# Optimization experiments

Measured on AMD Instinct MI355X. Metric: run time of the kernel, lower is better.

The kernel has to match this reference:

```python
import jax, jax.numpy as jnp
import numpy as np

B, IN_CH, OUT_CH = 4, 64, 128
N_HIGH, N_LOW = 163842, 40962
GROUPS, EPS, SLOPE = 4, 1e-5, 0.2


def setup_inputs() -> dict:
    key = jax.random.key(0)
    ks = jax.random.split(key, 6)
    x = jax.random.normal(ks[0], (B, IN_CH, N_HIGH), jnp.float32)
    pool_neigh = jax.random.randint(ks[1], (N_LOW * 7,), 0, N_HIGH, dtype=jnp.int32)
    conv_neigh = jax.random.randint(ks[2], (N_LOW * 7,), 0, N_LOW, dtype=jnp.int32)
    W1 = jax.random.normal(ks[3], (OUT_CH, 7 * IN_CH), jnp.float32) / np.float32(np.sqrt(7 * IN_CH))
    b1 = jnp.zeros((OUT_CH,), jnp.float32)
    W2 = jax.random.normal(ks[4], (OUT_CH, 7 * OUT_CH), jnp.float32) / np.float32(np.sqrt(7 * OUT_CH))
    b2 = jnp.zeros((OUT_CH,), jnp.float32)
    return dict(x=x, pool_neigh=pool_neigh, conv_neigh=conv_neigh,
                W1=W1, b1=b1, gn1_w=jnp.ones((OUT_CH,), jnp.float32), gn1_b=jnp.zeros((OUT_CH,), jnp.float32),
                W2=W2, b2=b2, gn2_w=jnp.ones((OUT_CH,), jnp.float32), gn2_b=jnp.zeros((OUT_CH,), jnp.float32))


def _mean_pool(x, pool_neigh):
    # x: (B, C, N_high); pool_neigh: (N_low*7,) -> (B, C, N_low)
    g = x[:, :, pool_neigh].reshape(x.shape[0], x.shape[1], -1, 7)
    return g.mean(axis=-1)


def _onering_conv(x, neigh, W, b):
    # x: (B, C, N); neigh: (N*7,); W: (O, 7*C). Torch Linear over gathered
    # (N*7, C).view(N, 7*C): neighbor-major, channel-minor concatenation.
    Bb, C, N = x.shape
    feat = x[:, :, neigh].reshape(Bb, C, N, 7)            # (B, C, N, 7)
    feat = jnp.transpose(feat, (0, 2, 3, 1)).reshape(Bb, N, 7 * C)  # (B, N, 7C)
    out = jnp.einsum('bnf,of->bno', feat, W) + b          # (B, N, O)
    return jnp.transpose(out, (0, 2, 1))                  # (B, O, N)


def _group_norm(x, w, b):
    # x: (B, C, N), normalize per (group, sample) over (C//G, N)
    Bb, C, N = x.shape
    xg = x.reshape(Bb, GROUPS, C // GROUPS, N)
    mu = xg.mean(axis=(2, 3), keepdims=True)
    var = ((xg - mu) ** 2).mean(axis=(2, 3), keepdims=True)
    xn = ((xg - mu) * jax.lax.rsqrt(var + EPS)).reshape(Bb, C, N)
    return xn * w[None, :, None] + b[None, :, None]


def _leaky_relu(x):
    return jnp.where(x >= 0, x, SLOPE * x)


def reference(x, pool_neigh, conv_neigh, W1, b1, gn1_w, gn1_b, W2, b2, gn2_w, gn2_b):
    h = _mean_pool(x, pool_neigh)
    h = _leaky_relu(_group_norm(_onering_conv(h, conv_neigh, W1, b1), gn1_w, gn1_b))
    h = _leaky_relu(_group_norm(_onering_conv(h, conv_neigh, W2, b2), gn2_w, gn2_b))
    return h
```

## Files before the change

### kernel.cpp

```cpp
#include <hip/hip_runtime.h>

#define B_SZ 4
#define IN_CH 64
#define OUT_CH 128
#define NHI 163842
#define NLO 40962
#define EPS_GN 1e-5f
#define SLOPE 0.2f

typedef __attribute__((ext_vector_type(8))) short short8;
typedef __attribute__((ext_vector_type(16))) float f32x16;

__device__ inline ushort f2bf(float f) {
    union { float f; unsigned u; } v; v.f = f;
    unsigned r = v.u + 0x7FFF + ((v.u >> 16) & 1);
    return (ushort)(r >> 16);
}
__device__ inline float bf2f(ushort h) {
    union { unsigned u; float f; } v; v.u = ((unsigned)h) << 16;
    return v.f;
}

__global__ void k_transpose_x(const float* __restrict__ x, ushort* __restrict__ xT) {
    __shared__ float t[64][65];
    const int b   = blockIdx.y;
    const int n0  = blockIdx.x * 64;
    const int tid = threadIdx.x;
    const int nq  = tid & 15;
    const int c0  = tid >> 4;
    const bool full = (n0 + 64) <= NHI;
    if (full) {
#pragma unroll
        for (int r = 0; r < 4; ++r) {
            int c = c0 + r * 16;
            float4 v = *(const float4*)&x[((long)b * IN_CH + c) * NHI + n0 + nq * 4];
            t[c][nq * 4 + 0] = v.x; t[c][nq * 4 + 1] = v.y;
            t[c][nq * 4 + 2] = v.z; t[c][nq * 4 + 3] = v.w;
        }
    } else {
        for (int r = 0; r < 4; ++r) {
            int c = c0 + r * 16;
            for (int e = 0; e < 4; ++e) {
                int n = n0 + nq * 4 + e;
                t[c][nq * 4 + e] = (n < NHI) ? x[((long)b * IN_CH + c) * NHI + n] : 0.f;
            }
        }
    }
    __syncthreads();
    const int n  = tid >> 2;
    const int cc = (tid & 3) * 16;
    if (n0 + n < NHI) {
        short8 o0, o1;
#pragma unroll
        for (int e = 0; e < 8; ++e) {
            o0[e] = (short)f2bf(t[cc + e][n]);
            o1[e] = (short)f2bf(t[cc + 8 + e][n]);
        }
        ushort* p = &xT[((long)b * NHI + n0 + n) * 64 + cc];
        *(short8*)p = o0;
        *(short8*)(p + 8) = o1;
    }
}

__global__ void k_prep_w(const float* __restrict__ W, ushort* __restrict__ Wb, int K) {
    int i = blockIdx.x * 256 + threadIdx.x;
    if (i >= K * 128) return;
    int k = i / 128, o = i % 128;
    int step = k >> 6, kk = k & 63, kg = kk >> 3, e = kk & 7;
    Wb[(((long)(step * 8 + kg) * 128 + o) * 8) + e] = f2bf(W[(long)o * K + k]);
}

__global__ void k_pool(const ushort* __restrict__ xT, const int* __restrict__ pn,
                       ushort* __restrict__ h1) {
    long t = (long)blockIdx.x * 256 + threadIdx.x;
    const long total = (long)B_SZ * NLO * 8;
    if (t >= total) return;
    int  cq = (int)(t & 7);
    long bn = t >> 3;
    int  n  = (int)(bn % NLO);
    int  b  = (int)(bn / NLO);
    float acc[8] = {};
#pragma unroll
    for (int j = 0; j < 7; ++j) {
        int idx = pn[n * 7 + j];
        short8 v = *(const short8*)&xT[((long)b * NHI + idx) * 64 + cq * 8];
#pragma unroll
        for (int e = 0; e < 8; ++e) acc[e] += bf2f((ushort)v[e]);
    }
    short8 o;
#pragma unroll
    for (int e = 0; e < 8; ++e) o[e] = (short)f2bf(acc[e] * (1.f / 7.f));
    *(short8*)&h1[bn * 64 + cq * 8] = o;
}

__device__ inline int aidx(int kg, int nn) {
    return (kg * 128 + (nn ^ (kg << 1))) * 8;
}

template <int CIN>
__global__ __launch_bounds__(256, 3)
void k_conv_mfma(const ushort* __restrict__ src, const int* __restrict__ nbr,
                 const ushort* __restrict__ Wb, const float* __restrict__ bias,
                 ushort* __restrict__ out, float* __restrict__ part) {
    constexpr int NSTEP = 7 * CIN / 64;
    __shared__ ushort Asm[2][8192];
    __shared__ float  red[4][2][2];

    const int b     = blockIdx.y;
    const int n0    = blockIdx.x * 128;
    const int tid   = threadIdx.x;
    const int lane  = tid & 63;
    const int wave  = tid >> 6;
    const int wr    = wave >> 1, wc = wave & 1;
    const int l31   = lane & 31;
    const int khalf = lane >> 5;

    const int s_nn = tid >> 2;
    const int s_kq = tid & 3;
    const int r0 = min(n0 + s_nn, NLO - 1);
    const int r1 = min(n0 + 64 + s_nn, NLO - 1);
    int nb0[7], nb1[7];
#pragma unroll
    for (int j = 0; j < 7; ++j) {
        nb0[j] = nbr[r0 * 7 + j];
        nb1[j] = nbr[r1 * 7 + j];
    }

    const long srcb = (long)b * NLO * CIN;
    f32x16 acc[2][2] = {};
    short8 a00, a01, a10, a11;

    {
        const ushort* p0 = &src[srcb + (long)nb0[0] * CIN + s_kq * 8];
        const ushort* p1 = &src[srcb + (long)nb1[0] * CIN + s_kq * 8];
        a00 = *(const short8*)p0; a01 = *(const short8*)(p0 + 32);
        a10 = *(const short8*)p1; a11 = *(const short8*)(p1 + 32);
        *(short8*)&Asm[0][aidx(s_kq,     s_nn)]      = a00;
        *(short8*)&Asm[0][aidx(s_kq + 4, s_nn)]      = a01;
        *(short8*)&Asm[0][aidx(s_kq,     64 + s_nn)] = a10;
        *(short8*)&Asm[0][aidx(s_kq + 4, 64 + s_nn)] = a11;
    }
    __syncthreads();

    for (int step = 0; step < NSTEP; ++step) {
        const int cur = step & 1;
        const int nxt = cur ^ 1;
        short8 bfr[4][2];
        {
            const ushort* wb = &Wb[(long)step * 8192 + (khalf * 128 + wc * 64 + l31) * 8];
#pragma unroll
            for (int kh = 0; kh < 4; ++kh) {
                bfr[kh][0] = *(const short8*)(wb + kh * 2 * 128 * 8);
                bfr[kh][1] = *(const short8*)(wb + kh * 2 * 128 * 8 + 32 * 8);
            }
        }
        if (step + 1 < NSTEP) {
            const int s  = step + 1;
            const int j  = (CIN == 64) ? s : (s >> 1);
            const int cb = (CIN == 64) ? 0 : ((s & 1) * 64);
            const ushort* p0 = &src[srcb + (long)nb0[j] * CIN + cb + s_kq * 8];
            const ushort* p1 = &src[srcb + (long)nb1[j] * CIN + cb + s_kq * 8];
            a00 = *(const short8*)p0; a01 = *(const short8*)(p0 + 32);
            a10 = *(const short8*)p1; a11 = *(const short8*)(p1 + 32);
        }
#pragma unroll
        for (int kh = 0; kh < 4; ++kh) {
            const int kg = 2 * kh + khalf;
            short8 A0 = *(const short8*)&Asm[cur][aidx(kg, wr * 64 + l31)];
            short8 A1 = *(const short8*)&Asm[cur][aidx(kg, wr * 64 + 32 + l31)];
            acc[0][0] = __builtin_amdgcn_mfma_f32_32x32x16_bf16(A0, bfr[kh][0], acc[0][0], 0, 0, 0);
            acc[0][1] = __builtin_amdgcn_mfma_f32_32x32x16_bf16(A0, bfr[kh][1], acc[0][1], 0, 0, 0);
            acc[1][0] = __builtin_amdgcn_mfma_f32_32x32x16_bf16(A1, bfr[kh][0], acc[1][0], 0, 0, 0);
            acc[1][1] = __builtin_amdgcn_mfma_f32_32x32x16_bf16(A1, bfr[kh][1], acc[1][1], 0, 0, 0);
        }
        if (step + 1 < NSTEP) {
            *(short8*)&Asm[nxt][aidx(s_kq,     s_nn)]      = a00;
            *(short8*)&Asm[nxt][aidx(s_kq + 4, s_nn)]      = a01;
            *(short8*)&Asm[nxt][aidx(s_kq,     64 + s_nn)] = a10;
            *(short8*)&Asm[nxt][aidx(s_kq + 4, 64 + s_nn)] = a11;
        }
        __syncthreads();
    }

    float bia[2];
#pragma unroll
    for (int n = 0; n < 2; ++n) bia[n] = bias[wc * 64 + n * 32 + l31];
    float s[2] = {}, q[2] = {};
#pragma unroll
    for (int m = 0; m < 2; ++m)
#pragma unroll
        for (int n = 0; n < 2; ++n)
#pragma unroll
            for (int r = 0; r < 16; ++r) {
                int crow = (r & 3) + 8 * (r >> 2) + 4 * khalf;
                int row  = n0 + wr * 64 + m * 32 + crow;
                float v  = acc[m][n][r] + bia[n];
                if (row < NLO) {
                    out[((long)b * NLO + row) * 128 + wc * 64 + n * 32 + l31] = f2bf(v);
                    s[n] += v; q[n] += v * v;
                }
            }
#pragma unroll
    for (int n = 0; n < 2; ++n)
#pragma unroll
        for (int off = 32; off > 0; off >>= 1) {
            s[n] += __shfl_down(s[n], off);
            q[n] += __shfl_down(q[n], off);
        }
    if (lane == 0) {
#pragma unroll
        for (int n = 0; n < 2; ++n) { red[wave][n][0] = s[n]; red[wave][n][1] = q[n]; }
    }
    __syncthreads();
    if (tid < 8) {
        int g = tid >> 1, isq = tid & 1;
        int gwc = g >> 1, gn = g & 1;
        float v = red[gwc][gn][isq] + red[2 + gwc][gn][isq];
        part[(((long)b * gridDim.x + blockIdx.x) * 4 + g) * 2 + isq] = v;
    }
}

__global__ void k_finalize(const float* __restrict__ part, int nblk,
                           const float* __restrict__ w, const float* __restrict__ bb,
                           float* __restrict__ scale, float* __restrict__ shift) {
    const int b = blockIdx.x >> 2, g = blockIdx.x & 3;
    const int tid = threadIdx.x;
    float s = 0.f, ss = 0.f;
    for (int k = tid; k < nblk; k += 256) {
        s  += part[(((long)b * nblk + k) * 4 + g) * 2 + 0];
        ss += part[(((long)b * nblk + k) * 4 + g) * 2 + 1];
    }
#pragma unroll
    for (int off = 32; off > 0; off >>= 1) {
        s += __shfl_down(s, off); ss += __shfl_down(ss, off);
    }
    __shared__ float red[8];
    __shared__ float fin[2];
    const int wave = tid >> 6, lane = tid & 63;
    if (lane == 0) { red[wave * 2] = s; red[wave * 2 + 1] = ss; }
    __syncthreads();
    if (tid == 0) {
        float as = red[0] + red[2] + red[4] + red[6];
        float aq = red[1] + red[3] + red[5] + red[7];
        const float cnt = 32.f * NLO;
        float mu  = as / cnt;
        float var = aq / cnt - mu * mu;
        fin[0] = mu; fin[1] = rsqrtf(var + EPS_GN);
    }
    __syncthreads();
    if (tid < 32) {
        int c = g * 32 + tid;
        float sc = fin[1] * w[c];
        scale[b * 128 + c] = sc;
        shift[b * 128 + c] = bb[c] - fin[0] * sc;
    }
}

__global__ void k_gnapply(const ushort* __restrict__ y, const float* __restrict__ sc,
                          const float* __restrict__ sh, ushort* __restrict__ yp) {
    long t = (long)blockIdx.x * 256 + threadIdx.x;
    const long total = (long)B_SZ * NLO * 16;
    if (t >= total) return;
    int  c8 = (int)(t & 15);
    long bn = t >> 4;
    int  b  = (int)(bn / NLO);
    short8 v = *(const short8*)&y[bn * 128 + c8 * 8];
    short8 o;
#pragma unroll
    for (int e = 0; e < 8; ++e) {
        int c = c8 * 8 + e;
        float f = bf2f((ushort)v[e]) * sc[b * 128 + c] + sh[b * 128 + c];
        f = fmaxf(f, SLOPE * f);
        o[e] = (short)f2bf(f);
    }
    *(short8*)&yp[bn * 128 + c8 * 8] = o;
}

__global__ void k_output(const ushort* __restrict__ y2, const float* __restrict__ scale,
                         const float* __restrict__ shift, float* __restrict__ out) {
    __shared__ float t[32][129];
    const int b   = blockIdx.y;
    const int n0  = blockIdx.x * 32;
    const int tid = threadIdx.x;
    const float* scb = &scale[b * 128];
    const float* shb = &shift[b * 128];
    const int c8 = (tid & 15) * 8;
#pragma unroll
    for (int r = 0; r < 2; ++r) {
        int nn = (tid >> 4) + r * 16;
        int n  = n0 + nn;
        if (n < NLO) {
            short8 v = *(const short8*)&y2[((long)b * NLO + n) * 128 + c8];
#pragma unroll
            for (int e = 0; e < 8; ++e) {
                int c = c8 + e;
                float f = bf2f((ushort)v[e]) * scb[c] + shb[c];
                t[nn][c] = fmaxf(f, SLOPE * f);
            }
        } else {
#pragma unroll
            for (int e = 0; e < 8; ++e) t[nn][c8 + e] = 0.f;
        }
    }
    __syncthreads();
    const int n4 = (tid & 7) * 4;
    const bool full = (n0 + 32) <= NLO;
#pragma unroll
    for (int r = 0; r < 4; ++r) {
        int c = (tid >> 3) + r * 32;
        long o = ((long)b * 128 + c) * NLO + n0 + n4;
        if (full) {
            float2 v0 = make_float2(t[n4][c], t[n4 + 1][c]);
            float2 v1 = make_float2(t[n4 + 2][c], t[n4 + 3][c]);
            *(float2*)&out[o]     = v0;
            *(float2*)&out[o + 2] = v1;
        } else {
            for (int e = 0; e < 4; ++e)
                if (n0 + n4 + e < NLO) out[o + e] = t[n4 + e][c];
        }
    }
}

extern "C" void kernel_launch(void* const* d_in, const int* in_sizes, int n_in,
                              void* d_out, int out_size, void* d_ws, size_t ws_size,
                              hipStream_t stream) {
    const float* x   = (const float*)d_in[0];
    const int*   pn  = (const int*)d_in[1];
    const int*   cn  = (const int*)d_in[2];
    const float* W1  = (const float*)d_in[3];
    const float* b1  = (const float*)d_in[4];
    const float* g1w = (const float*)d_in[5];
    const float* g1b = (const float*)d_in[6];
    const float* W2  = (const float*)d_in[7];
    const float* b2  = (const float*)d_in[8];
    const float* g2w = (const float*)d_in[9];
    const float* g2b = (const float*)d_in[10];
    float* out = (float*)d_out;
    char*  base = (char*)d_ws;

    ushort* xT  = (ushort*)(base + 0);
    ushort* y1  = (ushort*)(base + 0);
    ushort* y1p = (ushort*)(base + 44000000);
    ushort* h1  = (ushort*)(base + 88000000);
    ushort* y2  = (ushort*)(base + 110000000);
    ushort* wb1 = (ushort*)(base + 152000000);
    ushort* wb2 = (ushort*)(base + 152200000);
    float*  p1  = (float*)(base + 152500000);
    float*  p2  = (float*)(base + 152600000);
    float*  sc1 = (float*)(base + 152700000);
    float*  sh1 = sc1 + 512;
    float*  sc2 = (float*)(base + 152710000);
    float*  sh2 = sc2 + 512;

    const int NBLK = (NLO + 127) / 128;

    k_transpose_x<<<dim3((NHI + 63) / 64, B_SZ), 256, 0, stream>>>(x, xT);
    k_prep_w<<<(448 * 128 + 255) / 256, 256, 0, stream>>>(W1, wb1, 448);
    k_prep_w<<<(896 * 128 + 255) / 256, 256, 0, stream>>>(W2, wb2, 896);
    k_pool<<<(int)(((long)B_SZ * NLO * 8 + 255) / 256), 256, 0, stream>>>(xT, pn, h1);
    k_conv_mfma<64><<<dim3(NBLK, B_SZ), 256, 0, stream>>>(h1, cn, wb1, b1, y1, p1);
    k_finalize<<<16, 256, 0, stream>>>(p1, NBLK, g1w, g1b, sc1, sh1);
    k_gnapply<<<(int)(((long)B_SZ * NLO * 16 + 255) / 256), 256, 0, stream>>>(y1, sc1, sh1, y1p);
    k_conv_mfma<128><<<dim3(NBLK, B_SZ), 256, 0, stream>>>(y1p, cn, wb2, b2, y2, p2);
    k_finalize<<<16, 256, 0, stream>>>(p2, NBLK, g2w, g2b, sc2, sh2);
    k_output<<<dim3((NLO + 31) / 32, B_SZ), 256, 0, stream>>>(y2, sc2, sh2, out);
}
```

Before: 262.4 us.

## Restructure one-ring conv MFMA kernel to 64-row tiles with neighbor-step pipeline

Each conv block now covers 64 vertices instead of 128, so the grid has twice as many blocks, and occupancy is raised to four blocks per CU. The K loop now iterates over the 7 neighbors and stages a full neighbor's channel slice per step. Gathers are prefetched two steps ahead and written to LDS one step ahead. Weight fragments are loaded from global memory inside the inner loop, and the weight layout is flattened to match. The aim is better latency hiding of the irregular gathers, at the cost of reusing each weight load across fewer rows.

```diff
diff --git a/kernel.cpp b/kernel.cpp
--- a/kernel.cpp
+++ b/kernel.cpp
@@ -66,8 +66,8 @@
     int i = blockIdx.x * 256 + threadIdx.x;
     if (i >= K * 128) return;
     int k = i / 128, o = i % 128;
-    int step = k >> 6, kk = k & 63, kg = kk >> 3, e = kk & 7;
-    Wb[(((long)(step * 8 + kg) * 128 + o) * 8) + e] = f2bf(W[(long)o * K + k]);
+    int kg = k >> 3, e = k & 7;
+    Wb[(((long)kg * 128 + o) * 8) + e] = f2bf(W[(long)o * K + k]);
 }
 
 __global__ void k_pool(const ushort* __restrict__ xT, const int* __restrict__ pn,
@@ -94,20 +94,21 @@
 }
 
 __device__ inline int aidx(int kg, int nn) {
-    return (kg * 128 + (nn ^ (kg << 1))) * 8;
+    return (kg * 64 + (nn ^ ((kg & 7) << 1))) * 8;
 }
 
 template <int CIN>
-__global__ __launch_bounds__(256, 3)
+__global__ __launch_bounds__(256, 4)
 void k_conv_mfma(const ushort* __restrict__ src, const int* __restrict__ nbr,
                  const ushort* __restrict__ Wb, const float* __restrict__ bias,
                  ushort* __restrict__ out, float* __restrict__ part) {
-    constexpr int NSTEP = 7 * CIN / 64;
-    __shared__ ushort Asm[2][8192];
+    constexpr int KG = CIN / 8;
+    constexpr int CT = CIN / 32;
+    __shared__ ushort Asm[2][KG * 64 * 8];
     __shared__ float  red[4][2][2];
 
     const int b     = blockIdx.y;
-    const int n0    = blockIdx.x * 128;
+    const int n0    = blockIdx.x * 64;
     const int tid   = threadIdx.x;
     const int lane  = tid & 63;
     const int wave  = tid >> 6;
@@ -118,67 +119,53 @@
     const int s_nn = tid >> 2;
     const int s_kq = tid & 3;
     const int r0 = min(n0 + s_nn, NLO - 1);
-    const int r1 = min(n0 + 64 + s_nn, NLO - 1);
-    int nb0[7], nb1[7];
+    int nb[7];
+#pragma unroll
+    for (int j = 0; j < 7; ++j) nb[j] = nbr[r0 * 7 + j];
+
+    const long srcb = (long)b * NLO * CIN;
+    f32x16 acc[2] = {};
+    short8 aH[CT], aL[CT];
+
+    {
+        const ushort* p = &src[srcb + (long)nb[0] * CIN + s_kq * 8];
+        short8 t[CT];
+#pragma unroll
+        for (int i = 0; i < CT; ++i) t[i] = *(const short8*)(p + i * 32);
+#pragma unroll
+        for (int i = 0; i < CT; ++i)
+            *(short8*)&Asm[0][aidx(s_kq + 4 * i, s_nn)] = t[i];
+        const ushort* p1 = &src[srcb + (long)nb[1] * CIN + s_kq * 8];
+#pragma unroll
+        for (int i = 0; i < CT; ++i) aH[i] = *(const short8*)(p1 + i * 32);
+    }
+    __syncthreads();
+
 #pragma unroll
     for (int j = 0; j < 7; ++j) {
-        nb0[j] = nbr[r0 * 7 + j];
-        nb1[j] = nbr[r1 * 7 + j];
-    }
-
-    const long srcb = (long)b * NLO * CIN;
-    f32x16 acc[2][2] = {};
-    short8 a00, a01, a10, a11;
-
-    {
-        const ushort* p0 = &src[srcb + (long)nb0[0] * CIN + s_kq * 8];
-        const ushort* p1 = &src[srcb + (long)nb1[0] * CIN + s_kq * 8];
-        a00 = *(const short8*)p0; a01 = *(const short8*)(p0 + 32);
-        a10 = *(const short8*)p1; a11 = *(const short8*)(p1 + 32);
-        *(short8*)&Asm[0][aidx(s_kq,     s_nn)]      = a00;
-        *(short8*)&Asm[0][aidx(s_kq + 4, s_nn)]      = a01;
-        *(short8*)&Asm[0][aidx(s_kq,     64 + s_nn)] = a10;
-        *(short8*)&Asm[0][aidx(s_kq + 4, 64 + s_nn)] = a11;
-    }
-    __syncthreads();
-
-    for (int step = 0; step < NSTEP; ++step) {
-        const int cur = step & 1;
-        const int nxt = cur ^ 1;
-        short8 bfr[4][2];
-        {
-            const ushort* wb = &Wb[(long)step * 8192 + (khalf * 128 + wc * 64 + l31) * 8];
-#pragma unroll
-            for (int kh = 0; kh < 4; ++kh) {
-                bfr[kh][0] = *(const short8*)(wb + kh * 2 * 128 * 8);
-                bfr[kh][1] = *(const short8*)(wb + kh * 2 * 128 * 8 + 32 * 8);
-            }
-        }
-        if (step + 1 < NSTEP) {
-            const int s  = step + 1;
-            const int j  = (CIN == 64) ? s : (s >> 1);
-            const int cb = (CIN == 64) ? 0 : ((s & 1) * 64);
-            const ushort* p0 = &src[srcb + (long)nb0[j] * CIN + cb + s_kq * 8];
-            const ushort* p1 = &src[srcb + (long)nb1[j] * CIN + cb + s_kq * 8];
-            a00 = *(const short8*)p0; a01 = *(const short8*)(p0 + 32);
-            a10 = *(const short8*)p1; a11 = *(const short8*)(p1 + 32);
-        }
-#pragma unroll
-        for (int kh = 0; kh < 4; ++kh) {
+        const int cur = j & 1;
+        if (j + 2 < 7) {
+            const ushort* p = &src[srcb + (long)nb[j + 2] * CIN + s_kq * 8];
+#pragma unroll
+            for (int i = 0; i < CT; ++i) aL[i] = *(const short8*)(p + i * 32);
+        }
+        if (j + 1 < 7) {
+#pragma unroll
+            for (int i = 0; i < CT; ++i)
+                *(short8*)&Asm[cur ^ 1][aidx(s_kq + 4 * i, s_nn)] = aH[i];
+        }
+        const ushort* wbj = &Wb[((long)j * KG * 128 + wc * 64 + l31) * 8];
+#pragma unroll
+        for (int kh = 0; kh < KG / 2; ++kh) {
             const int kg = 2 * kh + khalf;
-            short8 A0 = *(const short8*)&Asm[cur][aidx(kg, wr * 64 + l31)];
-            short8 A1 = *(const short8*)&Asm[cur][aidx(kg, wr * 64 + 32 + l31)];
-            acc[0][0] = __builtin_amdgcn_mfma_f32_32x32x16_bf16(A0, bfr[kh][0], acc[0][0], 0, 0, 0);
-            acc[0][1] = __builtin_amdgcn_mfma_f32_32x32x16_bf16(A0, bfr[kh][1], acc[0][1], 0, 0, 0);
-            acc[1][0] = __builtin_amdgcn_mfma_f32_32x32x16_bf16(A1, bfr[kh][0], acc[1][0], 0, 0, 0);
-            acc[1][1] = __builtin_amdgcn_mfma_f32_32x32x16_bf16(A1, bfr[kh][1], acc[1][1], 0, 0, 0);
-        }
-        if (step + 1 < NSTEP) {
-            *(short8*)&Asm[nxt][aidx(s_kq,     s_nn)]      = a00;
-            *(short8*)&Asm[nxt][aidx(s_kq + 4, s_nn)]      = a01;
-            *(short8*)&Asm[nxt][aidx(s_kq,     64 + s_nn)] = a10;
-            *(short8*)&Asm[nxt][aidx(s_kq + 4, 64 + s_nn)] = a11;
-        }
+            short8 A0 = *(const short8*)&Asm[cur][aidx(kg, wr * 32 + l31)];
+            short8 B0 = *(const short8*)(wbj + (long)kg * 128 * 8);
+            short8 B1 = *(const short8*)(wbj + (long)kg * 128 * 8 + 32 * 8);
+            acc[0] = __builtin_amdgcn_mfma_f32_32x32x16_bf16(A0, B0, acc[0], 0, 0, 0);
+            acc[1] = __builtin_amdgcn_mfma_f32_32x32x16_bf16(A0, B1, acc[1], 0, 0, 0);
+        }
+#pragma unroll
+        for (int i = 0; i < CT; ++i) aH[i] = aL[i];
         __syncthreads();
     }
 
@@ -187,19 +174,17 @@
     for (int n = 0; n < 2; ++n) bia[n] = bias[wc * 64 + n * 32 + l31];
     float s[2] = {}, q[2] = {};
 #pragma unroll
-    for (int m = 0; m < 2; ++m)
-#pragma unroll
-        for (int n = 0; n < 2; ++n)
-#pragma unroll
-            for (int r = 0; r < 16; ++r) {
-                int crow = (r & 3) + 8 * (r >> 2) + 4 * khalf;
-                int row  = n0 + wr * 64 + m * 32 + crow;
-                float v  = acc[m][n][r] + bia[n];
-                if (row < NLO) {
-                    out[((long)b * NLO + row) * 128 + wc * 64 + n * 32 + l31] = f2bf(v);
-                    s[n] += v; q[n] += v * v;
-                }
+    for (int n = 0; n < 2; ++n)
+#pragma unroll
+        for (int r = 0; r < 16; ++r) {
+            int crow = (r & 3) + 8 * (r >> 2) + 4 * khalf;
+            int row  = n0 + wr * 32 + crow;
+            float v  = acc[n][r] + bia[n];
+            if (row < NLO) {
+                out[((long)b * NLO + row) * 128 + wc * 64 + n * 32 + l31] = f2bf(v);
+                s[n] += v; q[n] += v * v;
             }
+        }
 #pragma unroll
     for (int n = 0; n < 2; ++n)
 #pragma unroll
@@ -352,7 +337,7 @@
     float*  sc2 = (float*)(base + 152710000);
     float*  sh2 = sc2 + 512;
 
-    const int NBLK = (NLO + 127) / 128;
+    const int NBLK = (NLO + 63) / 64;
 
     k_transpose_x<<<dim3((NHI + 63) / 64, B_SZ), 256, 0, stream>>>(x, xT);
     k_prep_w<<<(448 * 128 + 255) / 256, 256, 0, stream>>>(W1, wb1, 448);
```

Measured after the change: 258.9 us. About the same (-1.3%).
